# Optimization experiments

Hardware: AMD Instinct MI355X
Metric: run time of the kernel (lower is better)

## Reference

```python
import jax, jax.numpy as jnp
import numpy as np

N, B, C, H = 900, 16, 256, 8
D = C // H
SCALE = D ** -0.5


def setup_inputs() -> dict:
    key = jax.random.key(0)
    ks = jax.random.split(key, 8)
    w = 0.02
    return {
        "query": jax.random.normal(ks[0], (N, B, C), dtype=jnp.float32),
        "key": jax.random.normal(ks[1], (N, B, C), dtype=jnp.float32),
        "value": jax.random.normal(ks[2], (N, B, C), dtype=jnp.float32),
        "prior_weight": jax.random.uniform(ks[3], (B, H, N, N), dtype=jnp.float32),
        "Wq": jax.random.normal(ks[4], (C, C), dtype=jnp.float32) * w,
        "bq": jnp.zeros((C,), dtype=jnp.float32),
        "Wk": jax.random.normal(ks[5], (C, C), dtype=jnp.float32) * w,
        "bk": jnp.zeros((C,), dtype=jnp.float32),
        "Wv": jax.random.normal(ks[6], (C, C), dtype=jnp.float32) * w,
        "bv": jnp.zeros((C,), dtype=jnp.float32),
        "Wo": jax.random.normal(ks[7], (C, C), dtype=jnp.float32) * w,
        "bo": jnp.zeros((C,), dtype=jnp.float32),
    }


def reference(query, key, value, prior_weight, Wq, bq, Wk, bk, Wv, bv, Wo, bo):
    # query/key/value: [N, B, C] (seq-first, batch_first=False)
    n, b, c = query.shape
    # projections (torch Linear: x @ W^T + b)
    q = query @ Wq.T + bq
    k = key @ Wk.T + bk
    v = value @ Wv.T + bv
    # [N,B,C] -> [B,H,N,D]
    to_bhnd = lambda t: jnp.transpose(t.reshape(n, b, H, D), (1, 2, 0, 3))
    q = to_bhnd(q) * SCALE
    k = to_bhnd(k)
    v = to_bhnd(v)
    # attention logits, elementwise prior multiply, softmax
    attn = jnp.einsum("bhnd,bhmd->bhnm", q, k) * prior_weight
    attn = jax.nn.softmax(attn, axis=-1)
    out = jnp.einsum("bhnm,bhmd->bhnd", attn, v)  # [B,H,N,D]
    out = jnp.transpose(out, (0, 2, 1, 3)).reshape(b, n, c)  # [B,N,C]
    return out @ Wo.T + bo
```

## Files before the change

### kernel.cpp

```cpp
#include <hip/hip_runtime.h>
#include <stdint.h>

#define NSEQ 900
#define CH 256
#define NH 8
#define HD 32
#define SCALE 0.17677669529663687f
#define VTP 912

typedef unsigned short u16;
typedef __attribute__((ext_vector_type(8))) short bf16x8;
typedef __attribute__((ext_vector_type(4))) float f32x4;

__device__ __forceinline__ uint32_t f2bf(float f) {
  uint32_t u = __float_as_uint(f);
  return (u + 0x7fffu + ((u >> 16) & 1u)) >> 16;
}

__device__ __forceinline__ uint4 pack8(float4 a, float4 b) {
  uint4 r;
  r.x = f2bf(a.x) | (f2bf(a.y) << 16);
  r.y = f2bf(a.z) | (f2bf(a.w) << 16);
  r.z = f2bf(b.x) | (f2bf(b.y) << 16);
  r.w = f2bf(b.z) | (f2bf(b.w) << 16);
  return r;
}

__global__ __launch_bounds__(256) void proj_qkv_kernel(
    const float* __restrict__ xq, const float* __restrict__ xk, const float* __restrict__ xv,
    const float* __restrict__ Wq, const float* __restrict__ Wk, const float* __restrict__ Wv,
    const float* __restrict__ bq, const float* __restrict__ bk, const float* __restrict__ bv,
    u16* __restrict__ Q, u16* __restrict__ K, u16* __restrict__ V) {
  __shared__ u16 smem[5120];
  const int t = threadIdx.x;
  const int r0 = blockIdx.x * 64, c0 = blockIdx.y * 64;
  const int mode = blockIdx.z;
  const float* X    = (mode == 0) ? xq : (mode == 1) ? xk : xv;
  const float* W    = (mode == 0) ? Wq : (mode == 1) ? Wk : Wv;
  const float* bias = (mode == 0) ? bq : (mode == 1) ? bk : bv;
  u16* OUT          = (mode == 0) ? Q  : (mode == 1) ? K  : V;

  const int lane = t & 63, wv = t >> 6;
  const int wr = (wv >> 1) * 32, wc = (wv & 1) * 32;
  const int lr = lane & 15, lq = lane >> 4;
  const int arow = t >> 2, akq = (t & 3) * 8;
  const float* Xr = X + (r0 + arow) * CH + akq;
  const float* Wr = W + (c0 + arow) * CH + akq;

  f32x4 acc[2][2];
#pragma unroll
  for (int i = 0; i < 2; ++i)
#pragma unroll
    for (int j = 0; j < 2; ++j) acc[i][j] = (f32x4){0.f, 0.f, 0.f, 0.f};

  for (int kc = 0; kc < CH; kc += 32) {
    const float4 a0 = *(const float4*)(Xr + kc);
    const float4 a1 = *(const float4*)(Xr + kc + 4);
    const float4 b0 = *(const float4*)(Wr + kc);
    const float4 b1 = *(const float4*)(Wr + kc + 4);
    __syncthreads();
    *(uint4*)&smem[arow * 40 + akq]        = pack8(a0, a1);
    *(uint4*)&smem[2560 + arow * 40 + akq] = pack8(b0, b1);
    __syncthreads();
    const bf16x8 af0 = *(const bf16x8*)&smem[(wr + lr) * 40 + lq * 8];
    const bf16x8 af1 = *(const bf16x8*)&smem[(wr + 16 + lr) * 40 + lq * 8];
    const bf16x8 bf0 = *(const bf16x8*)&smem[2560 + (wc + lr) * 40 + lq * 8];
    const bf16x8 bf1 = *(const bf16x8*)&smem[2560 + (wc + 16 + lr) * 40 + lq * 8];
    acc[0][0] = __builtin_amdgcn_mfma_f32_16x16x32_bf16(af0, bf0, acc[0][0], 0, 0, 0);
    acc[0][1] = __builtin_amdgcn_mfma_f32_16x16x32_bf16(af0, bf1, acc[0][1], 0, 0, 0);
    acc[1][0] = __builtin_amdgcn_mfma_f32_16x16x32_bf16(af1, bf0, acc[1][0], 0, 0, 0);
    acc[1][1] = __builtin_amdgcn_mfma_f32_16x16x32_bf16(af1, bf1, acc[1][1], 0, 0, 0);
  }

  __syncthreads();
  const float qs = (mode == 0) ? SCALE : 1.0f;
#pragma unroll
  for (int tr = 0; tr < 2; ++tr)
#pragma unroll
    for (int tc = 0; tc < 2; ++tc) {
      const int col = wc + tc * 16 + lr;
      const float bi = bias[c0 + col];
#pragma unroll
      for (int r = 0; r < 4; ++r) {
        const int row = wr + tr * 16 + lq * 4 + r;
        smem[row * 72 + col] = (u16)f2bf((acc[tr][tc][r] + bi) * qs);
      }
    }
  __syncthreads();

  const int n_base = r0 >> 4, h_base = c0 >> 5;
#pragma unroll
  for (int rep = 0; rep < 2; ++rep) {
    const int task = rep * 256 + t;
    const int d16 = task & 3, nl = (task >> 2) & 3, bhl = task >> 4;
    const int hl = bhl & 1, bb = bhl >> 1;
    const int lrow = nl * 16 + bb, lcol = hl * 32 + d16 * 8;
    const uint4 val = *(const uint4*)&smem[lrow * 72 + lcol];
    const size_t o = ((size_t)(bb * NH + h_base + hl) * NSEQ + n_base + nl) * HD + d16 * 8;
    *(uint4*)&OUT[o] = val;
  }
}

__global__ __launch_bounds__(256) void transpose_v_kernel(
    const u16* __restrict__ V, u16* __restrict__ Vt) {
  __shared__ u16 T[32][136];
  const int t = threadIdx.x;
  const int bh = blockIdx.y;
  const int n0 = blockIdx.x * 128;
  {
    const int i = t >> 1, dh = (t & 1) * 16;
    const int n = min(n0 + i, NSEQ - 1);
    const uint4 v0 = *(const uint4*)&V[((size_t)bh * NSEQ + n) * HD + dh];
    const uint4 v1 = *(const uint4*)&V[((size_t)bh * NSEQ + n) * HD + dh + 8];
    const u16* u = (const u16*)&v0;
#pragma unroll
    for (int j = 0; j < 8; ++j) T[dh + j][i] = u[j];
    const u16* u2 = (const u16*)&v1;
#pragma unroll
    for (int j = 0; j < 8; ++j) T[dh + 8 + j][i] = u2[j];
  }
  __syncthreads();
  const int d = t >> 3, nb = (t & 7) * 16;
  u16* dst = Vt + ((size_t)bh * HD + d) * VTP + n0 + nb;
  if (n0 + nb + 15 < NSEQ) {
    *(uint4*)dst       = *(const uint4*)&T[d][nb];
    *(uint4*)(dst + 8) = *(const uint4*)&T[d][nb + 8];
  } else {
#pragma unroll
    for (int j = 0; j < 16; ++j)
      if (n0 + nb + j < NSEQ) dst[j] = T[d][nb + j];
  }
}

__global__ __launch_bounds__(256) void attn_kernel(
    const u16* __restrict__ Q, const u16* __restrict__ K,
    const u16* __restrict__ Vt, const float* __restrict__ prior,
    u16* __restrict__ AO) {
  __shared__ u16 Plds[4][640];
  __shared__ float Ow[4][16][32];
  __shared__ float Lw[4][16];

  const int t = threadIdx.x;
  const int n0 = blockIdx.x * 16;
  const int bh = blockIdx.y;
  const int lane = t & 63, wv = t >> 6;
  const int lr = lane & 15, lq = lane >> 4;

  const u16* Qb = Q + (size_t)bh * NSEQ * HD;
  const u16* Kb = K + (size_t)bh * NSEQ * HD;
  const u16* Vb = Vt + (size_t)bh * HD * VTP;
  const float* Pb = prior + (size_t)bh * NSEQ * NSEQ;

  const int qrow = min(n0 + lr, NSEQ - 1);
  const bf16x8 qf = *(const bf16x8*)&Qb[qrow * HD + lq * 8];

  int nrow[4];
#pragma unroll
  for (int r = 0; r < 4; ++r) nrow[r] = min(n0 + lq * 4 + r, NSEQ - 1);

  f32x4 acc0 = {0.f, 0.f, 0.f, 0.f};
  f32x4 acc1 = {0.f, 0.f, 0.f, 0.f};
  float lpart[4] = {0.f, 0.f, 0.f, 0.f};

  u16* Pw = &Plds[wv][0];

  for (int c = wv; c < 29; c += 4) {
    const int m0 = c * 32;
    const int mA = m0 + lr, mB = m0 + 16 + lr;
    const bool vA = mA < NSEQ, vB = mB < NSEQ;
    const int mAc = min(mA, NSEQ - 1), mBc = min(mB, NSEQ - 1);
    const bf16x8 kf0 = *(const bf16x8*)&Kb[mAc * HD + lq * 8];
    const bf16x8 kf1 = *(const bf16x8*)&Kb[mBc * HD + lq * 8];
    const f32x4 z = {0.f, 0.f, 0.f, 0.f};
    f32x4 s0 = __builtin_amdgcn_mfma_f32_16x16x32_bf16(qf, kf0, z, 0, 0, 0);
    f32x4 s1 = __builtin_amdgcn_mfma_f32_16x16x32_bf16(qf, kf1, z, 0, 0, 0);

#pragma unroll
    for (int r = 0; r < 4; ++r) {
      const float pA = Pb[(size_t)nrow[r] * NSEQ + mAc];
      const float pB = Pb[(size_t)nrow[r] * NSEQ + mBc];
      const float e0 = vA ? __expf(s0[r] * pA) : 0.f;
      const float e1 = vB ? __expf(s1[r] * pB) : 0.f;
      lpart[r] += e0 + e1;
      Pw[(lq * 4 + r) * 40 + lr]      = (u16)f2bf(e0);
      Pw[(lq * 4 + r) * 40 + 16 + lr] = (u16)f2bf(e1);
    }
    const bf16x8 pf  = *(const bf16x8*)&Pw[lr * 40 + lq * 8];
    const bf16x8 vf0 = *(const bf16x8*)&Vb[lr * VTP + m0 + lq * 8];
    const bf16x8 vf1 = *(const bf16x8*)&Vb[(16 + lr) * VTP + m0 + lq * 8];
    acc0 = __builtin_amdgcn_mfma_f32_16x16x32_bf16(pf, vf0, acc0, 0, 0, 0);
    acc1 = __builtin_amdgcn_mfma_f32_16x16x32_bf16(pf, vf1, acc1, 0, 0, 0);
  }

#pragma unroll
  for (int off = 1; off < 16; off <<= 1)
#pragma unroll
    for (int r = 0; r < 4; ++r) lpart[r] += __shfl_xor(lpart[r], off);

#pragma unroll
  for (int r = 0; r < 4; ++r) {
    const int row = lq * 4 + r;
    Ow[wv][row][lr]      = acc0[r];
    Ow[wv][row][16 + lr] = acc1[r];
    if (lr == 0) Lw[wv][row] = lpart[r];
  }
  __syncthreads();
#pragma unroll
  for (int rep = 0; rep < 2; ++rep) {
    const int idx = rep * 256 + t;
    const int i = idx >> 5, d = idx & 31;
    const float num = Ow[0][i][d] + Ow[1][i][d] + Ow[2][i][d] + Ow[3][i][d];
    const float den = Lw[0][i] + Lw[1][i] + Lw[2][i] + Lw[3][i];
    const int n = n0 + i;
    if (n < NSEQ)
      AO[((size_t)(bh >> 3) * NSEQ + n) * CH + (bh & 7) * HD + d] = (u16)f2bf(num / den);
  }
}

__global__ __launch_bounds__(256) void proj_o_kernel(
    const u16* __restrict__ AO, const float* __restrict__ Wo,
    const float* __restrict__ bo, float* __restrict__ out) {
  __shared__ u16 As[64][40], Bs[64][40];
  const int t = threadIdx.x;
  const int r0 = blockIdx.x * 64, c0 = blockIdx.y * 64;
  const int lane = t & 63, wv = t >> 6;
  const int wr = (wv >> 1) * 32, wc = (wv & 1) * 32;
  const int lr = lane & 15, lq = lane >> 4;
  const int arow = t >> 2, akq = (t & 3) * 8;
  const u16* Ar = AO + (size_t)(r0 + arow) * CH + akq;
  const float* Wr = Wo + (c0 + arow) * CH + akq;

  f32x4 acc[2][2];
#pragma unroll
  for (int i = 0; i < 2; ++i)
#pragma unroll
    for (int j = 0; j < 2; ++j) acc[i][j] = (f32x4){0.f, 0.f, 0.f, 0.f};

  for (int kc = 0; kc < CH; kc += 32) {
    const uint4 ap = *(const uint4*)(Ar + kc);
    const float4 b0 = *(const float4*)(Wr + kc);
    const float4 b1 = *(const float4*)(Wr + kc + 4);
    __syncthreads();
    *(uint4*)&As[arow][akq] = ap;
    *(uint4*)&Bs[arow][akq] = pack8(b0, b1);
    __syncthreads();
    const bf16x8 af0 = *(const bf16x8*)&As[wr + lr][lq * 8];
    const bf16x8 af1 = *(const bf16x8*)&As[wr + 16 + lr][lq * 8];
    const bf16x8 bf0 = *(const bf16x8*)&Bs[wc + lr][lq * 8];
    const bf16x8 bf1 = *(const bf16x8*)&Bs[wc + 16 + lr][lq * 8];
    acc[0][0] = __builtin_amdgcn_mfma_f32_16x16x32_bf16(af0, bf0, acc[0][0], 0, 0, 0);
    acc[0][1] = __builtin_amdgcn_mfma_f32_16x16x32_bf16(af0, bf1, acc[0][1], 0, 0, 0);
    acc[1][0] = __builtin_amdgcn_mfma_f32_16x16x32_bf16(af1, bf0, acc[1][0], 0, 0, 0);
    acc[1][1] = __builtin_amdgcn_mfma_f32_16x16x32_bf16(af1, bf1, acc[1][1], 0, 0, 0);
  }
#pragma unroll
  for (int tr = 0; tr < 2; ++tr)
#pragma unroll
    for (int tc = 0; tc < 2; ++tc) {
      const int col = c0 + wc + tc * 16 + lr;
      const float bi = bo[col];
#pragma unroll
      for (int r = 0; r < 4; ++r) {
        const int row = r0 + wr + tr * 16 + lq * 4 + r;
        out[(size_t)row * CH + col] = acc[tr][tc][r] + bi;
      }
    }
}

extern "C" void kernel_launch(void* const* d_in, const int* in_sizes, int n_in,
                              void* d_out, int out_size, void* d_ws, size_t ws_size,
                              hipStream_t stream) {
  (void)in_sizes; (void)n_in; (void)out_size; (void)ws_size;
  const float* query = (const float*)d_in[0];
  const float* key_  = (const float*)d_in[1];
  const float* value = (const float*)d_in[2];
  const float* prior = (const float*)d_in[3];
  const float* Wq = (const float*)d_in[4];
  const float* bq = (const float*)d_in[5];
  const float* Wk = (const float*)d_in[6];
  const float* bk = (const float*)d_in[7];
  const float* Wv = (const float*)d_in[8];
  const float* bv = (const float*)d_in[9];
  const float* Wo = (const float*)d_in[10];
  const float* bo = (const float*)d_in[11];

  u16* wsu = (u16*)d_ws;
  const size_t SZ = (size_t)16 * NH * NSEQ * HD;
  const size_t SZT = (size_t)16 * NH * HD * VTP;
  u16* Q  = wsu;
  u16* K  = wsu + SZ;
  u16* V  = wsu + 2 * SZ;
  u16* Vt = wsu + 3 * SZ;
  u16* AO = Vt + SZT + 64;

  proj_qkv_kernel<<<dim3(225, 4, 3), 256, 0, stream>>>(
      query, key_, value, Wq, Wk, Wv, bq, bk, bv, Q, K, V);
  transpose_v_kernel<<<dim3(8, 128), 256, 0, stream>>>(V, Vt);
  attn_kernel<<<dim3(57, 128), 256, 0, stream>>>(Q, K, Vt, prior, AO);
  proj_o_kernel<<<dim3(225, 4), 256, 0, stream>>>(AO, Wo, bo, (float*)d_out);
}
```

Before: 689.7 us.

## Transpose QK MFMA so prior loads become contiguous float4 rows

Swaps the MFMA operand order for the score tile so each lane holds four consecutive key columns of one query row. The prior can then be read as float4 vectors along a row instead of scattered scalar loads, and the P tile is packed into LDS as bf16 pairs. The row-sum reduction shrinks to two shuffles. The partial last key chunk is peeled into a wave-0 epilogue so the main loop needs no bounds checks, and the Vt padding columns are now zero-filled. The risk is extra complexity in the tail path, and the main loop now has 28 chunks over 4 waves instead of 29.

```diff
diff --git a/kernel.cpp b/kernel.cpp
--- a/kernel.cpp
+++ b/kernel.cpp
@@ -1,4 +1,5 @@
 #include <hip/hip_runtime.h>
+#include <hip/hip_bf16.h>
 #include <stdint.h>
 
 #define NSEQ 900
@@ -15,6 +16,13 @@
 __device__ __forceinline__ uint32_t f2bf(float f) {
   uint32_t u = __float_as_uint(f);
   return (u + 0x7fffu + ((u >> 16) & 1u)) >> 16;
+}
+
+__device__ __forceinline__ uint32_t pkbf2(float a, float b) {
+  __hip_bfloat162 h = __float22bfloat162_rn(make_float2(a, b));
+  uint32_t u;
+  __builtin_memcpy(&u, &h, 4);
+  return u;
 }
 
 __device__ __forceinline__ uint4 pack8(float4 a, float4 b) {
@@ -127,8 +135,10 @@
     *(uint4*)(dst + 8) = *(const uint4*)&T[d][nb + 8];
   } else {
 #pragma unroll
-    for (int j = 0; j < 16; ++j)
-      if (n0 + nb + j < NSEQ) dst[j] = T[d][nb + j];
+    for (int j = 0; j < 16; ++j) {
+      const int col = n0 + nb + j;
+      if (col < VTP) dst[j] = (col < NSEQ) ? T[d][nb + j] : (u16)0;
+    }
   }
 }
 
@@ -153,38 +163,32 @@
 
   const int qrow = min(n0 + lr, NSEQ - 1);
   const bf16x8 qf = *(const bf16x8*)&Qb[qrow * HD + lq * 8];
-
-  int nrow[4];
-#pragma unroll
-  for (int r = 0; r < 4; ++r) nrow[r] = min(n0 + lq * 4 + r, NSEQ - 1);
+  const float* Prow = Pb + (size_t)qrow * NSEQ;
 
   f32x4 acc0 = {0.f, 0.f, 0.f, 0.f};
   f32x4 acc1 = {0.f, 0.f, 0.f, 0.f};
-  float lpart[4] = {0.f, 0.f, 0.f, 0.f};
-
+  float lsum = 0.f;
   u16* Pw = &Plds[wv][0];
 
-  for (int c = wv; c < 29; c += 4) {
+  for (int c = wv; c < 28; c += 4) {
     const int m0 = c * 32;
-    const int mA = m0 + lr, mB = m0 + 16 + lr;
-    const bool vA = mA < NSEQ, vB = mB < NSEQ;
-    const int mAc = min(mA, NSEQ - 1), mBc = min(mB, NSEQ - 1);
-    const bf16x8 kf0 = *(const bf16x8*)&Kb[mAc * HD + lq * 8];
-    const bf16x8 kf1 = *(const bf16x8*)&Kb[mBc * HD + lq * 8];
+    const bf16x8 kf0 = *(const bf16x8*)&Kb[(m0 + lr) * HD + lq * 8];
+    const bf16x8 kf1 = *(const bf16x8*)&Kb[(m0 + 16 + lr) * HD + lq * 8];
+    const float4 pA = *(const float4*)&Prow[m0 + lq * 4];
+    const float4 pB = *(const float4*)&Prow[m0 + 16 + lq * 4];
     const f32x4 z = {0.f, 0.f, 0.f, 0.f};
-    f32x4 s0 = __builtin_amdgcn_mfma_f32_16x16x32_bf16(qf, kf0, z, 0, 0, 0);
-    f32x4 s1 = __builtin_amdgcn_mfma_f32_16x16x32_bf16(qf, kf1, z, 0, 0, 0);
-
-#pragma unroll
-    for (int r = 0; r < 4; ++r) {
-      const float pA = Pb[(size_t)nrow[r] * NSEQ + mAc];
-      const float pB = Pb[(size_t)nrow[r] * NSEQ + mBc];
-      const float e0 = vA ? __expf(s0[r] * pA) : 0.f;
-      const float e1 = vB ? __expf(s1[r] * pB) : 0.f;
-      lpart[r] += e0 + e1;
-      Pw[(lq * 4 + r) * 40 + lr]      = (u16)f2bf(e0);
-      Pw[(lq * 4 + r) * 40 + 16 + lr] = (u16)f2bf(e1);
-    }
+    const f32x4 s0 = __builtin_amdgcn_mfma_f32_16x16x32_bf16(kf0, qf, z, 0, 0, 0);
+    const f32x4 s1 = __builtin_amdgcn_mfma_f32_16x16x32_bf16(kf1, qf, z, 0, 0, 0);
+    const float e0 = __expf(s0[0] * pA.x), e1 = __expf(s0[1] * pA.y);
+    const float e2 = __expf(s0[2] * pA.z), e3 = __expf(s0[3] * pA.w);
+    const float e4 = __expf(s1[0] * pB.x), e5 = __expf(s1[1] * pB.y);
+    const float e6 = __expf(s1[2] * pB.z), e7 = __expf(s1[3] * pB.w);
+    lsum += ((e0 + e1) + (e2 + e3)) + ((e4 + e5) + (e6 + e7));
+    uint2 w0, w1;
+    w0.x = pkbf2(e0, e1); w0.y = pkbf2(e2, e3);
+    w1.x = pkbf2(e4, e5); w1.y = pkbf2(e6, e7);
+    *(uint2*)&Pw[lr * 40 + lq * 4]      = w0;
+    *(uint2*)&Pw[lr * 40 + 16 + lq * 4] = w1;
     const bf16x8 pf  = *(const bf16x8*)&Pw[lr * 40 + lq * 8];
     const bf16x8 vf0 = *(const bf16x8*)&Vb[lr * VTP + m0 + lq * 8];
     const bf16x8 vf1 = *(const bf16x8*)&Vb[(16 + lr) * VTP + m0 + lq * 8];
@@ -192,18 +196,40 @@
     acc1 = __builtin_amdgcn_mfma_f32_16x16x32_bf16(pf, vf1, acc1, 0, 0, 0);
   }
 
-#pragma unroll
-  for (int off = 1; off < 16; off <<= 1)
-#pragma unroll
-    for (int r = 0; r < 4; ++r) lpart[r] += __shfl_xor(lpart[r], off);
+  if (wv == 0) {
+    const int m0 = 896;
+    const bf16x8 kf0 = *(const bf16x8*)&Kb[min(m0 + lr, NSEQ - 1) * HD + lq * 8];
+    const float4 pA = *(const float4*)&Prow[m0];
+    const f32x4 z = {0.f, 0.f, 0.f, 0.f};
+    const f32x4 s0 = __builtin_amdgcn_mfma_f32_16x16x32_bf16(kf0, qf, z, 0, 0, 0);
+    float e0 = 0.f, e1 = 0.f, e2 = 0.f, e3 = 0.f;
+    if (lq == 0) {
+      e0 = __expf(s0[0] * pA.x); e1 = __expf(s0[1] * pA.y);
+      e2 = __expf(s0[2] * pA.z); e3 = __expf(s0[3] * pA.w);
+    }
+    lsum += (e0 + e1) + (e2 + e3);
+    uint2 w0, w1;
+    w0.x = pkbf2(e0, e1); w0.y = pkbf2(e2, e3);
+    w1.x = 0u; w1.y = 0u;
+    *(uint2*)&Pw[lr * 40 + lq * 4]      = w0;
+    *(uint2*)&Pw[lr * 40 + 16 + lq * 4] = w1;
+    const bf16x8 pf  = *(const bf16x8*)&Pw[lr * 40 + lq * 8];
+    const bf16x8 vf0 = *(const bf16x8*)&Vb[lr * VTP + m0 + lq * 8];
+    const bf16x8 vf1 = *(const bf16x8*)&Vb[(16 + lr) * VTP + m0 + lq * 8];
+    acc0 = __builtin_amdgcn_mfma_f32_16x16x32_bf16(pf, vf0, acc0, 0, 0, 0);
+    acc1 = __builtin_amdgcn_mfma_f32_16x16x32_bf16(pf, vf1, acc1, 0, 0, 0);
+  }
+
+  lsum += __shfl_xor(lsum, 16);
+  lsum += __shfl_xor(lsum, 32);
 
 #pragma unroll
   for (int r = 0; r < 4; ++r) {
     const int row = lq * 4 + r;
     Ow[wv][row][lr]      = acc0[r];
     Ow[wv][row][16 + lr] = acc1[r];
-    if (lr == 0) Lw[wv][row] = lpart[r];
-  }
+  }
+  if (lane < 16) Lw[wv][lane] = lsum;
   __syncthreads();
 #pragma unroll
   for (int rep = 0; rep < 2; ++rep) {
```

Result: faster. 675.6 us (-2.0%).
